# Optimization experiments

Measured on AMD Instinct MI355X. Metric: run time of the kernel, lower is better.

Reference implementation:

```python
import jax, jax.numpy as jnp
import numpy as np

SIGMA = 0.1
B, C, H, W = 2, 3, 64, 64


def setup_inputs() -> dict:
    key = jax.random.key(0)
    x = jax.random.uniform(key, (B, C, H, W), dtype=jnp.float32)
    return {"x": x}


def reference(x) -> jnp.ndarray:
    """Range-only bilateral filter: out[p] = sum_q K(p,q) x[q] / sum_q K(p,q),
    K(p,q) = exp(-((x_q - x_p)/sigma)^2), all-pairs over the H*W pixels,
    independently per (batch, channel)."""
    b, c, h, w = x.shape
    n = h * w
    xf = x.reshape(b, c, n)                      # [B,C,N]
    # pairwise intensity differences -> Gaussian range kernel [B,C,N,N]
    diff = xf[:, :, :, None] - xf[:, :, None, :]
    K = jnp.exp(-jnp.square(diff / SIGMA))
    num = jnp.einsum('bcpq,bcq->bcp', K, xf)     # weighted sum over source pixels
    den = jnp.sum(K, axis=-1)                    # normalization
    return (num / den).reshape(b, c, h, w)
```

## Files before the change

kernel.cpp:

```cpp
#include <hip/hip_runtime.h>

#define NSLICE 6
#define NPIX   4096
#define M      20
#define TPB    512

#define C0         0.088622693f
#define TWO_C0     0.177245385f
#define AEXP_LOG2  0.035597112f
#define DEN0       362.99854f

__global__ __launch_bounds__(TPB) void bilateral_fused(
        const float* __restrict__ x, float* __restrict__ out) {
    __shared__ float4 part4[32][4][5];
    __shared__ float  xpart[32];
    __shared__ __align__(16) float fin[(M + 1) * 4];

    const int tid = threadIdx.x;
    const int s   = blockIdx.x >> 3;
    const int bt  = blockIdx.x & 7;
    const float* xs = x + s * NPIX;

    const int fg  = tid & 3;
    const int set = tid >> 2;
    const float a = (float)(5 * fg);

    float Sc[5], Ss[5], Tc[5], Ts[5], X = 0.f;
    #pragma unroll
    for (int k = 0; k < 5; ++k) { Sc[k]=0.f; Ss[k]=0.f; Tc[k]=0.f; Ts[k]=0.f; }

    const float4* x4 = (const float4*)xs;
    #pragma unroll
    for (int j = 0; j < 8; ++j) {
        float4 v4 = x4[set * 8 + j];
        float vv[4] = {v4.x, v4.y, v4.z, v4.w};
        #pragma unroll
        for (int u = 0; u < 4; ++u) {
            float v = vv[u];
            X += v;
            float h  = 0.5f * v;
            float c1 = __builtin_amdgcn_cosf(h);
            float tc = c1 + c1;
            float cp = __builtin_amdgcn_cosf(a * h);
            float sp = __builtin_amdgcn_sinf(a * h);
            float cc = __builtin_amdgcn_cosf(fmaf(a, h, h));
            float ss = __builtin_amdgcn_sinf(fmaf(a, h, h));
            #pragma unroll
            for (int k = 0; k < 5; ++k) {
                Sc[k] += cc;  Ss[k] += ss;
                Tc[k] = fmaf(v, cc, Tc[k]);  Ts[k] = fmaf(v, ss, Ts[k]);
                float cn = fmaf(tc, cc, -cp);
                float sn = fmaf(tc, ss, -sp);
                cp = cc; cc = cn; sp = ss; ss = sn;
            }
        }
    }

    #pragma unroll
    for (int off = 4; off <= 8; off <<= 1) {
        X += __shfl_xor(X, off);
        #pragma unroll
        for (int k = 0; k < 5; ++k) {
            Sc[k] += __shfl_xor(Sc[k], off);
            Ss[k] += __shfl_xor(Ss[k], off);
            Tc[k] += __shfl_xor(Tc[k], off);
            Ts[k] += __shfl_xor(Ts[k], off);
        }
    }
    const int lane = tid & 63;
    const int wv   = tid >> 6;
    if ((lane & 12) == 0) {
        int g = (wv << 2) | (lane >> 4);
        #pragma unroll
        for (int k = 0; k < 5; ++k)
            part4[g][fg][k] = make_float4(Sc[k], Ss[k], Tc[k], Ts[k]);
        if ((lane & 15) == 0) xpart[g] = X;
    }
    __syncthreads();

    if (tid < 81) {
        if (tid == 80) {
            float xx = 0.f;
            #pragma unroll
            for (int g = 0; g < 32; ++g) xx += xpart[g];
            fin[0] = DEN0;  fin[1] = C0 * xx;  fin[2] = 0.f;  fin[3] = 0.f;
        } else {
            const float* pf = (const float*)part4;
            float sum = 0.f;
            #pragma unroll
            for (int g = 0; g < 32; ++g) sum += pf[g * 80 + tid];
            int m = (tid >> 2) + 1;
            float fm = (float)m;
            float coef = TWO_C0 * __builtin_amdgcn_exp2f(-AEXP_LOG2 * fm * fm);
            fin[m * 4 + (tid & 3)] = coef * sum;
        }
    }
    __syncthreads();

    const int p = bt * TPB + tid;
    float v  = xs[p];
    float h  = 0.5f * v;
    float s1 = __builtin_amdgcn_sinf(h);
    float c1 = __builtin_amdgcn_cosf(h);
    const float4* F = (const float4*)fin;
    float4 f0 = F[0], f1 = F[1];
    float den = fmaf(c1, f1.x, f0.x);  den = fmaf(s1, f1.y, den);
    float num = fmaf(c1, f1.z, f0.y);  num = fmaf(s1, f1.w, num);
    float tc = c1 + c1, cm2 = 1.f, sm2 = 0.f, cm1 = c1, sm1 = s1;
    #pragma unroll
    for (int m = 2; m <= M; ++m) {
        float cn = fmaf(tc, cm1, -cm2);
        float sn = fmaf(tc, sm1, -sm2);
        cm2 = cm1; cm1 = cn; sm2 = sm1; sm1 = sn;
        float4 f = F[m];
        den = fmaf(cn, f.x, den);  den = fmaf(sn, f.y, den);
        num = fmaf(cn, f.z, num);  num = fmaf(sn, f.w, num);
    }
    out[s * NPIX + p] = num / den;
}

extern "C" void kernel_launch(void* const* d_in, const int* in_sizes, int n_in,
                              void* d_out, int out_size, void* d_ws, size_t ws_size,
                              hipStream_t stream) {
    const float* x = (const float*)d_in[0];
    float* out = (float*)d_out;
    bilateral_fused<<<dim3(NSLICE * 8), dim3(TPB), 0, stream>>>(x, out);
}
```

Measured before the change: 56.86 us.

## Split Fourier harmonics into two groups of ten and reduce fully within wavefronts

Each thread now accumulates ten harmonics instead of five, with two frequency groups per pixel set. The second group's start angle comes from one sin/cos plus an angle-addition identity, which cuts transcendental calls per pixel. The cross-lane reduction now runs over the whole wavefront, so LDS partials shrink from 32 groups to 8 and the final sum gets shorter. In exchange, per-thread register use roughly doubles, there is a divergent branch on fg within each wave, and the shuffle reduction takes more steps.

New measurement: 59.80 us. 1.05x slower.

```diff
diff --git a/kernel.cpp b/kernel.cpp
--- a/kernel.cpp
+++ b/kernel.cpp
@@ -10,10 +10,10 @@
 #define AEXP_LOG2  0.035597112f
 #define DEN0       362.99854f
 
-__global__ __launch_bounds__(TPB) void bilateral_fused(
+__global__ __launch_bounds__(TPB) void bilateral_fused2(
         const float* __restrict__ x, float* __restrict__ out) {
-    __shared__ float4 part4[32][4][5];
-    __shared__ float  xpart[32];
+    __shared__ float4 part4[8][2][10];
+    __shared__ float  xpart[8];
     __shared__ __align__(16) float fin[(M + 1) * 4];
 
     const int tid = threadIdx.x;
@@ -21,32 +21,39 @@
     const int bt  = blockIdx.x & 7;
     const float* xs = x + s * NPIX;
 
-    const int fg  = tid & 3;
-    const int set = tid >> 2;
-    const float a = (float)(5 * fg);
+    const int fg  = tid & 1;
+    const int set = tid >> 1;
 
-    float Sc[5], Ss[5], Tc[5], Ts[5], X = 0.f;
+    float Sc[10], Ss[10], Tc[10], Ts[10], X = 0.f;
     #pragma unroll
-    for (int k = 0; k < 5; ++k) { Sc[k]=0.f; Ss[k]=0.f; Tc[k]=0.f; Ts[k]=0.f; }
+    for (int k = 0; k < 10; ++k) { Sc[k]=0.f; Ss[k]=0.f; Tc[k]=0.f; Ts[k]=0.f; }
 
     const float4* x4 = (const float4*)xs;
     #pragma unroll
-    for (int j = 0; j < 8; ++j) {
-        float4 v4 = x4[set * 8 + j];
+    for (int j = 0; j < 4; ++j) {
+        float4 v4 = x4[set * 4 + j];
         float vv[4] = {v4.x, v4.y, v4.z, v4.w};
         #pragma unroll
         for (int u = 0; u < 4; ++u) {
             float v = vv[u];
-            X += v;
             float h  = 0.5f * v;
             float c1 = __builtin_amdgcn_cosf(h);
+            float s1 = __builtin_amdgcn_sinf(h);
             float tc = c1 + c1;
-            float cp = __builtin_amdgcn_cosf(a * h);
-            float sp = __builtin_amdgcn_sinf(a * h);
-            float cc = __builtin_amdgcn_cosf(fmaf(a, h, h));
-            float ss = __builtin_amdgcn_sinf(fmaf(a, h, h));
+            float cp, sp, cc, ss;
+            if (fg == 0) {
+                X += v;
+                cp = 1.f;  sp = 0.f;
+                cc = c1;   ss = s1;
+            } else {
+                float cA = __builtin_amdgcn_cosf(10.f * h);
+                float sA = __builtin_amdgcn_sinf(10.f * h);
+                cp = cA;  sp = sA;
+                cc = fmaf(cA, c1, -(sA * s1));
+                ss = fmaf(sA, c1,  (cA * s1));
+            }
             #pragma unroll
-            for (int k = 0; k < 5; ++k) {
+            for (int k = 0; k < 10; ++k) {
                 Sc[k] += cc;  Ss[k] += ss;
                 Tc[k] = fmaf(v, cc, Tc[k]);  Ts[k] = fmaf(v, ss, Ts[k]);
                 float cn = fmaf(tc, cc, -cp);
@@ -57,10 +64,10 @@
     }
 
     #pragma unroll
-    for (int off = 4; off <= 8; off <<= 1) {
+    for (int off = 2; off < 64; off <<= 1) {
         X += __shfl_xor(X, off);
         #pragma unroll
-        for (int k = 0; k < 5; ++k) {
+        for (int k = 0; k < 10; ++k) {
             Sc[k] += __shfl_xor(Sc[k], off);
             Ss[k] += __shfl_xor(Ss[k], off);
             Tc[k] += __shfl_xor(Tc[k], off);
@@ -69,12 +76,11 @@
     }
     const int lane = tid & 63;
     const int wv   = tid >> 6;
-    if ((lane & 12) == 0) {
-        int g = (wv << 2) | (lane >> 4);
+    if (lane < 2) {
         #pragma unroll
-        for (int k = 0; k < 5; ++k)
-            part4[g][fg][k] = make_float4(Sc[k], Ss[k], Tc[k], Ts[k]);
-        if ((lane & 15) == 0) xpart[g] = X;
+        for (int k = 0; k < 10; ++k)
+            part4[wv][fg][k] = make_float4(Sc[k], Ss[k], Tc[k], Ts[k]);
+        if (lane == 0) xpart[wv] = X;
     }
     __syncthreads();
 
@@ -82,13 +88,13 @@
         if (tid == 80) {
             float xx = 0.f;
             #pragma unroll
-            for (int g = 0; g < 32; ++g) xx += xpart[g];
+            for (int g = 0; g < 8; ++g) xx += xpart[g];
             fin[0] = DEN0;  fin[1] = C0 * xx;  fin[2] = 0.f;  fin[3] = 0.f;
         } else {
             const float* pf = (const float*)part4;
             float sum = 0.f;
             #pragma unroll
-            for (int g = 0; g < 32; ++g) sum += pf[g * 80 + tid];
+            for (int g = 0; g < 8; ++g) sum += pf[g * 80 + tid];
             int m = (tid >> 2) + 1;
             float fm = (float)m;
             float coef = TWO_C0 * __builtin_amdgcn_exp2f(-AEXP_LOG2 * fm * fm);
@@ -124,5 +130,5 @@
                               hipStream_t stream) {
     const float* x = (const float*)d_in[0];
     float* out = (float*)d_out;
-    bilateral_fused<<<dim3(NSLICE * 8), dim3(TPB), 0, stream>>>(x, out);
+    bilateral_fused2<<<dim3(NSLICE * 8), dim3(TPB), 0, stream>>>(x, out);
 }
```
